# Performance work log

Measured on AMD Instinct MI355X. Metric: run time of the kernel, lower is better.

## Reference

```python
import jax, jax.numpy as jnp
import numpy as np

N, D, K = 32768, 128, 32
EPS = 1e-8  # torch.cosine_similarity default eps


def setup_inputs() -> dict:
    key = jax.random.key(0)
    k1, k2, k3, k4, k5 = jax.random.split(key, 5)
    # xavier_normal_ std = sqrt(2/(fan_in+fan_out)); torch treats dims (-2,-1) as (fan_in, fan_out)
    std_w = (2.0 / (D + D)) ** 0.5
    std_v = (2.0 / (2 * D + 1)) ** 0.5
    return {
        "x_1": jax.random.normal(k1, (N, D), dtype=jnp.float32),
        "x_2": jax.random.normal(k2, (N, D), dtype=jnp.float32),
        "W1": jax.random.normal(k3, (K, D, D), dtype=jnp.float32) * std_w,
        "W2": jax.random.normal(k4, (K, D, D), dtype=jnp.float32) * std_w,
        "V": jax.random.normal(k5, (K, 2 * D, 1), dtype=jnp.float32) * std_v,
        "b": jnp.zeros((K,), dtype=jnp.float32),
    }


def reference(x_1, x_2, W1, W2, V, b):
    # Batched bilinear transforms: [N, K, D]
    x1t = jnp.einsum("nd,kde->nke", x_1, W1)
    x2t = jnp.einsum("nd,kde->nke", x_2, W2)
    # Cosine similarity along last dim (torch semantics: clamp norms at eps)
    dot = jnp.sum(x1t * x2t, axis=-1)                     # [N, K]
    n1 = jnp.maximum(jnp.linalg.norm(x1t, axis=-1), EPS)  # [N, K]
    n2 = jnp.maximum(jnp.linalg.norm(x2t, axis=-1), EPS)
    part1 = dot / (n1 * n2)
    # part2 = cat([x1, x2]) @ V[k]  -> [N, K]
    xcat = jnp.concatenate([x_1, x_2], axis=-1)           # [N, 2D]
    part2 = jnp.einsum("nf,kf->nk", xcat, V[:, :, 0])
    return jax.nn.relu(part1 + part2 + b)
```

## Files before the change

kernel.cpp:

```cpp
#include <hip/hip_runtime.h>
#include <cstdint>
#include <cstddef>

#define DD 128
#define KK 32
constexpr float EPS = 1e-8f;

typedef __bf16 bf16x8 __attribute__((ext_vector_type(8)));
typedef float f32x4 __attribute__((ext_vector_type(4)));

__device__ __forceinline__ unsigned short f2bf(float x) {
    union { float f; uint32_t u; } v; v.f = x;
    uint32_t r = v.u + 0x7FFFu + ((v.u >> 16) & 1u);
    return (unsigned short)(r >> 16);
}
__device__ __forceinline__ __bf16 f2bf16(float x) {
    unsigned short u = f2bf(x);
    __bf16 r; __builtin_memcpy(&r, &u, 2); return r;
}
__device__ __forceinline__ uint4 pack8(float4 a, float4 b) {
    uint4 o;
    o.x = (uint32_t)f2bf(a.x) | ((uint32_t)f2bf(a.y) << 16);
    o.y = (uint32_t)f2bf(a.z) | ((uint32_t)f2bf(a.w) << 16);
    o.z = (uint32_t)f2bf(b.x) | ((uint32_t)f2bf(b.y) << 16);
    o.w = (uint32_t)f2bf(b.z) | ((uint32_t)f2bf(b.w) << 16);
    return o;
}

template <int CTRL>
__device__ __forceinline__ float dpp_fold(float x) {
    union { float f; int i; } u, r;
    u.f = x;
    r.i = __builtin_amdgcn_update_dpp(0, u.i, CTRL, 0xF, 0xF, false);
    return x + r.f;
}
__device__ __forceinline__ f32x4 fold4(f32x4 v) {
    #pragma unroll
    for (int c = 0; c < 4; ++c) {
        float x = v[c];
        x = dpp_fold<0xB1>(x);
        x = dpp_fold<0x4E>(x);
        v[c] = x;
    }
    return v;
}

__global__ __launch_bounds__(256) void prep_kernel(
    const float* __restrict__ x1, const float* __restrict__ x2,
    const float* __restrict__ W1, const float* __restrict__ W2,
    __bf16* __restrict__ X1f, __bf16* __restrict__ X2f,
    __bf16* __restrict__ W1f, __bf16* __restrict__ W2f,
    int cvt_half, int wf_half)
{
    __shared__ float tile[16][132];
    int bb = blockIdx.x;
    if (bb < 2 * cvt_half) {
        const float* src; __bf16* dst;
        if (bb >= cvt_half) { src = x2; dst = X2f; bb -= cvt_half; }
        else                { src = x1; dst = X1f; }
        const int rg = bb;
        {
            const int row = threadIdx.x >> 4;
            const int c8  = (threadIdx.x & 15) * 8;
            const float* p = src + (size_t)(rg * 16 + row) * DD + c8;
            float4 f0 = *reinterpret_cast<const float4*>(p);
            float4 f1 = *reinterpret_cast<const float4*>(p + 4);
            *reinterpret_cast<float4*>(&tile[row][c8])     = f0;
            *reinterpret_cast<float4*>(&tile[row][c8 + 4]) = f1;
        }
        __syncthreads();
        {
            const int mm = threadIdx.x & 15;
            const int c  = threadIdx.x >> 4;
            float4 a = *reinterpret_cast<float4*>(&tile[mm][c * 8]);
            float4 b = *reinterpret_cast<float4*>(&tile[mm][c * 8 + 4]);
            size_t off = (size_t)rg * 2048 + (size_t)c * 128 + (size_t)mm * 8;
            *reinterpret_cast<uint4*>(dst + off) = pack8(a, b);
        }
    } else {
        bb -= 2 * cvt_half;
        const float* W; __bf16* Wf;
        if (bb >= wf_half) { W = W2; Wf = W2f; bb -= wf_half; }
        else               { W = W1; Wf = W1f; }
        int idx = bb * 256 + threadIdx.x;
        int mm = idx & 15;
        int c  = (idx >> 4) & 15;
        int eg = (idx >> 8) & 7;
        int k  = idx >> 11;
        const float* Wk = W + (size_t)k * DD * DD;
        int e = eg * 16 + mm;
        float4 a, b;
        a.x = Wk[(size_t)(c * 8 + 0) * DD + e];
        a.y = Wk[(size_t)(c * 8 + 1) * DD + e];
        a.z = Wk[(size_t)(c * 8 + 2) * DD + e];
        a.w = Wk[(size_t)(c * 8 + 3) * DD + e];
        b.x = Wk[(size_t)(c * 8 + 4) * DD + e];
        b.y = Wk[(size_t)(c * 8 + 5) * DD + e];
        b.z = Wk[(size_t)(c * 8 + 6) * DD + e];
        b.w = Wk[(size_t)(c * 8 + 7) * DD + e];
        size_t off = ((size_t)(k * 8 + eg)) * 2048 + (size_t)c * 128 + (size_t)mm * 8;
        *reinterpret_cast<uint4*>(Wf + off) = pack8(a, b);
    }
}

__global__ __launch_bounds__(256) void part2_kernel(
    const __bf16* __restrict__ X1f, const __bf16* __restrict__ X2f,
    const float* __restrict__ V, float* __restrict__ p2w) {
    const int wave = threadIdx.x >> 6, lane = threadIdx.x & 63;
    const int m = lane & 15, quad = lane >> 4;
    const int rg0 = blockIdx.x * 16 + wave * 4;

    f32x4 acc[4][2];
    #pragma unroll
    for (int rt = 0; rt < 4; ++rt)
        #pragma unroll
        for (int ct = 0; ct < 2; ++ct) acc[rt][ct] = f32x4{0.f, 0.f, 0.f, 0.f};

    #pragma unroll
    for (int ks = 0; ks < 8; ++ks) {
        const __bf16* Xs = (ks < 4) ? X1f : X2f;
        const int kss = ks & 3;
        bf16x8 a[4];
        #pragma unroll
        for (int rt = 0; rt < 4; ++rt)
            a[rt] = *reinterpret_cast<const bf16x8*>(
                Xs + (size_t)(rg0 + rt) * 2048 + kss * 512 + lane * 8);
        #pragma unroll
        for (int ct = 0; ct < 2; ++ct) {
            const float* p = V + (size_t)(ct * 16 + m) * 256 + ks * 32 + quad * 8;
            float4 v0 = *reinterpret_cast<const float4*>(p);
            float4 v1 = *reinterpret_cast<const float4*>(p + 4);
            bf16x8 b;
            b[0] = f2bf16(v0.x); b[1] = f2bf16(v0.y); b[2] = f2bf16(v0.z); b[3] = f2bf16(v0.w);
            b[4] = f2bf16(v1.x); b[5] = f2bf16(v1.y); b[6] = f2bf16(v1.z); b[7] = f2bf16(v1.w);
            #pragma unroll
            for (int rt = 0; rt < 4; ++rt)
                acc[rt][ct] = __builtin_amdgcn_mfma_f32_16x16x32_bf16(a[rt], b, acc[rt][ct], 0, 0, 0);
        }
    }
    const int row0 = blockIdx.x * 256 + wave * 64;
    #pragma unroll
    for (int rt = 0; rt < 4; ++rt)
        #pragma unroll
        for (int ct = 0; ct < 2; ++ct)
            #pragma unroll
            for (int reg = 0; reg < 4; ++reg)
                p2w[(size_t)(row0 + rt * 16 + quad * 4 + reg) * KK + ct * 16 + m] = acc[rt][ct][reg];
}

__global__ __launch_bounds__(256, 2) void ntn_main(
    const __bf16* __restrict__ X1f, const __bf16* __restrict__ X2f,
    const __bf16* __restrict__ W1f, const __bf16* __restrict__ W2f,
    const float* __restrict__ p2w, const float* __restrict__ bias,
    float* __restrict__ out, int grp_per_xcd)
{
    __shared__ __align__(16) float sRedAll[8][3][2][4][40];

    const int b    = blockIdx.x;
    const int xcd  = b & 7;
    const int k    = (b >> 3) & 31;
    const int grpN = xcd * grp_per_xcd + (b >> 8);
    const int tid  = threadIdx.x;
    const int wave = tid >> 6;
    const int lane = tid & 63;
    const int m    = lane & 15;
    const int quad = lane >> 4;
    const int rh   = wave & 1;
    const int eh   = wave >> 1;

    const size_t nOut = (size_t)grpN * 256 + tid;
    const float p2v = p2w[nOut * KK + k];
    const float bk  = bias[k];

    const __bf16* W1p = W1f + (size_t)k * 16384;
    const __bf16* W2p = W2f + (size_t)k * 16384;

    bf16x8 Bc[2][4][4];
    #pragma unroll
    for (int ks = 0; ks < 4; ++ks)
        #pragma unroll
        for (int et = 0; et < 4; ++et) {
            const size_t boff = (size_t)(eh * 4 + et) * 2048 + ks * 512 + lane * 8;
            Bc[0][ks][et] = *reinterpret_cast<const bf16x8*>(W1p + boff);
            Bc[1][ks][et] = *reinterpret_cast<const bf16x8*>(W2p + boff);
        }

    const int rg0 = grpN * 16;
    const size_t lane8 = (size_t)lane * 8;

    bf16x8 a1[4], a2[4];
    {
        const size_t ab = (size_t)(rg0 + rh) * 2048 + lane8;
        #pragma unroll
        for (int ks = 0; ks < 4; ++ks) {
            a1[ks] = *reinterpret_cast<const bf16x8*>(X1f + ab + ks * 512);
            a2[ks] = *reinterpret_cast<const bf16x8*>(X2f + ab + ks * 512);
        }
    }

    #pragma unroll
    for (int g = 0; g < 8; ++g) {
        f32x4 acc[2][4];
        #pragma unroll
        for (int mat = 0; mat < 2; ++mat)
            #pragma unroll
            for (int et = 0; et < 4; ++et) acc[mat][et] = f32x4{0.f, 0.f, 0.f, 0.f};

        #pragma unroll
        for (int ks = 0; ks < 4; ++ks) {
            #pragma unroll
            for (int et = 0; et < 4; ++et) {
                acc[0][et] = __builtin_amdgcn_mfma_f32_16x16x32_bf16(a1[ks], Bc[0][ks][et], acc[0][et], 0, 0, 0);
                acc[1][et] = __builtin_amdgcn_mfma_f32_16x16x32_bf16(a2[ks], Bc[1][ks][et], acc[1][et], 0, 0, 0);
            }
        }

        if (g < 7) {
            const size_t ab = (size_t)(rg0 + (g + 1) * 2 + rh) * 2048 + lane8;
            #pragma unroll
            for (int ks = 0; ks < 4; ++ks) {
                a1[ks] = *reinterpret_cast<const bf16x8*>(X1f + ab + ks * 512);
                a2[ks] = *reinterpret_cast<const bf16x8*>(X2f + ab + ks * 512);
            }
        }

        f32x4 pd = {0.f, 0.f, 0.f, 0.f};
        f32x4 q1 = {0.f, 0.f, 0.f, 0.f};
        f32x4 q2 = {0.f, 0.f, 0.f, 0.f};
        #pragma unroll
        for (int et = 0; et < 4; ++et) {
            f32x4 c1 = acc[0][et];
            f32x4 c2 = acc[1][et];
            pd += c1 * c2;
            q1 += c1 * c1;
            q2 += c2 * c2;
        }
        pd = fold4(pd);
        q1 = fold4(q1);
        q2 = fold4(q2);

        if ((m & 3) == 0) {
            const int grp = m >> 2;
            const int rb  = rh * 16 + quad * 4;
            *reinterpret_cast<f32x4*>(&sRedAll[g][0][eh][grp][rb]) = pd;
            *reinterpret_cast<f32x4*>(&sRedAll[g][1][eh][grp][rb]) = q1;
            *reinterpret_cast<f32x4*>(&sRedAll[g][2][eh][grp][rb]) = q2;
        }
    }

    __syncthreads();

    {
        const int tile = tid >> 5;
        const int row  = tid & 31;
        float dot = 0.f, s1 = 0.f, s2 = 0.f;
        #pragma unroll
        for (int e2 = 0; e2 < 2; ++e2)
            #pragma unroll
            for (int gg = 0; gg < 4; ++gg) {
                dot += sRedAll[tile][0][e2][gg][row];
                s1  += sRedAll[tile][1][e2][gg][row];
                s2  += sRedAll[tile][2][e2][gg][row];
            }
        float n1 = fmaxf(sqrtf(s1), EPS);
        float n2 = fmaxf(sqrtf(s2), EPS);
        float tot = dot / (n1 * n2) + p2v + bk;
        out[nOut * KK + k] = fmaxf(tot, 0.f);
    }
}

extern "C" void kernel_launch(void* const* d_in, const int* in_sizes, int n_in,
                              void* d_out, int out_size, void* d_ws, size_t ws_size,
                              hipStream_t stream) {
    const float* x1 = (const float*)d_in[0];
    const float* x2 = (const float*)d_in[1];
    const float* W1 = (const float*)d_in[2];
    const float* W2 = (const float*)d_in[3];
    const float* V  = (const float*)d_in[4];
    const float* b  = (const float*)d_in[5];
    float* out = (float*)d_out;

    const int N = in_sizes[0] / DD;

    __bf16* X1f = (__bf16*)d_ws;
    __bf16* X2f = X1f + (size_t)N * DD;
    __bf16* W1f = X2f + (size_t)N * DD;
    __bf16* W2f = W1f + (size_t)KK * DD * DD;
    float*  p2w = (float*)(W2f + (size_t)KK * DD * DD);

    const int cvt_half = N / 16;
    const int wf_half  = KK * DD * DD / 8 / 256;
    prep_kernel<<<2 * cvt_half + 2 * wf_half, 256, 0, stream>>>(
        x1, x2, W1, W2, X1f, X2f, W1f, W2f, cvt_half, wf_half);

    part2_kernel<<<N / 256, 256, 0, stream>>>(X1f, X2f, V, p2w);

    const int groups = N / 256;
    ntn_main<<<groups * KK, 256, 0, stream>>>(X1f, X2f, W1f, W2f, p2w, b, out,
                                              groups / 8);
}
```

Measured before the change: 170.0 us.

## Fold part2 GEMV into prep kernel and raise MFMA wave priority

Removes the separate bf16 MFMA part2 kernel and computes the x·V projection as an fp32 GEMV inside the prep kernel, using extra blocks that read the raw fp32 inputs. This saves one kernel launch and removes the dependency of part2 on the bf16 conversion. The trade-off is that x1/x2 are now read twice in fp32 within prep and the GEMV runs on scalar FMAs instead of MFMA. Separately, it wraps the main kernel's MFMA loop in s_setprio to favour waves that are issuing matrix work.

```diff
diff --git a/kernel.cpp b/kernel.cpp
--- a/kernel.cpp
+++ b/kernel.cpp
@@ -13,10 +13,6 @@
     union { float f; uint32_t u; } v; v.f = x;
     uint32_t r = v.u + 0x7FFFu + ((v.u >> 16) & 1u);
     return (unsigned short)(r >> 16);
-}
-__device__ __forceinline__ __bf16 f2bf16(float x) {
-    unsigned short u = f2bf(x);
-    __bf16 r; __builtin_memcpy(&r, &u, 2); return r;
 }
 __device__ __forceinline__ uint4 pack8(float4 a, float4 b) {
     uint4 o;
@@ -48,20 +44,54 @@
 __global__ __launch_bounds__(256) void prep_kernel(
     const float* __restrict__ x1, const float* __restrict__ x2,
     const float* __restrict__ W1, const float* __restrict__ W2,
+    const float* __restrict__ V,  float* __restrict__ p2w,
     __bf16* __restrict__ X1f, __bf16* __restrict__ X2f,
     __bf16* __restrict__ W1f, __bf16* __restrict__ W2f,
-    int cvt_half, int wf_half)
+    int ngemv, int cvt_half, int wf_half)
 {
     __shared__ float tile[16][132];
+    __shared__ float xrow[8][260];
+
     int bb = blockIdx.x;
+    const int tid = threadIdx.x;
+
+    if (bb < ngemv) {
+        const int rb = bb * 8;
+        #pragma unroll
+        for (int i = 0; i < 2; ++i) {
+            int idx = tid + i * 256;
+            int row = idx >> 6;
+            int col = idx & 63;
+            const float* src = (col < 32)
+                ? (x1 + (size_t)(rb + row) * DD + col * 4)
+                : (x2 + (size_t)(rb + row) * DD + (col - 32) * 4);
+            *reinterpret_cast<float4*>(&xrow[row][col * 4]) =
+                *reinterpret_cast<const float4*>(src);
+        }
+        __syncthreads();
+        const int k   = tid & 31;
+        const int row = tid >> 5;
+        const float* Vk = V + (size_t)k * 256;
+        float acc = 0.f;
+        #pragma unroll 8
+        for (int c = 0; c < 64; ++c) {
+            float4 v  = *reinterpret_cast<const float4*>(Vk + c * 4);
+            float4 xv = *reinterpret_cast<const float4*>(&xrow[row][c * 4]);
+            acc += xv.x * v.x + xv.y * v.y + xv.z * v.z + xv.w * v.w;
+        }
+        p2w[(size_t)(rb + row) * KK + k] = acc;
+        return;
+    }
+    bb -= ngemv;
+
     if (bb < 2 * cvt_half) {
         const float* src; __bf16* dst;
         if (bb >= cvt_half) { src = x2; dst = X2f; bb -= cvt_half; }
         else                { src = x1; dst = X1f; }
         const int rg = bb;
         {
-            const int row = threadIdx.x >> 4;
-            const int c8  = (threadIdx.x & 15) * 8;
+            const int row = tid >> 4;
+            const int c8  = (tid & 15) * 8;
             const float* p = src + (size_t)(rg * 16 + row) * DD + c8;
             float4 f0 = *reinterpret_cast<const float4*>(p);
             float4 f1 = *reinterpret_cast<const float4*>(p + 4);
@@ -70,8 +100,8 @@
         }
         __syncthreads();
         {
-            const int mm = threadIdx.x & 15;
-            const int c  = threadIdx.x >> 4;
+            const int mm = tid & 15;
+            const int c  = tid >> 4;
             float4 a = *reinterpret_cast<float4*>(&tile[mm][c * 8]);
             float4 b = *reinterpret_cast<float4*>(&tile[mm][c * 8 + 4]);
             size_t off = (size_t)rg * 2048 + (size_t)c * 128 + (size_t)mm * 8;
@@ -82,7 +112,7 @@
         const float* W; __bf16* Wf;
         if (bb >= wf_half) { W = W2; Wf = W2f; bb -= wf_half; }
         else               { W = W1; Wf = W1f; }
-        int idx = bb * 256 + threadIdx.x;
+        int idx = bb * 256 + tid;
         int mm = idx & 15;
         int c  = (idx >> 4) & 15;
         int eg = (idx >> 8) & 7;
@@ -103,51 +133,6 @@
     }
 }
 
-__global__ __launch_bounds__(256) void part2_kernel(
-    const __bf16* __restrict__ X1f, const __bf16* __restrict__ X2f,
-    const float* __restrict__ V, float* __restrict__ p2w) {
-    const int wave = threadIdx.x >> 6, lane = threadIdx.x & 63;
-    const int m = lane & 15, quad = lane >> 4;
-    const int rg0 = blockIdx.x * 16 + wave * 4;
-
-    f32x4 acc[4][2];
-    #pragma unroll
-    for (int rt = 0; rt < 4; ++rt)
-        #pragma unroll
-        for (int ct = 0; ct < 2; ++ct) acc[rt][ct] = f32x4{0.f, 0.f, 0.f, 0.f};
-
-    #pragma unroll
-    for (int ks = 0; ks < 8; ++ks) {
-        const __bf16* Xs = (ks < 4) ? X1f : X2f;
-        const int kss = ks & 3;
-        bf16x8 a[4];
-        #pragma unroll
-        for (int rt = 0; rt < 4; ++rt)
-            a[rt] = *reinterpret_cast<const bf16x8*>(
-                Xs + (size_t)(rg0 + rt) * 2048 + kss * 512 + lane * 8);
-        #pragma unroll
-        for (int ct = 0; ct < 2; ++ct) {
-            const float* p = V + (size_t)(ct * 16 + m) * 256 + ks * 32 + quad * 8;
-            float4 v0 = *reinterpret_cast<const float4*>(p);
-            float4 v1 = *reinterpret_cast<const float4*>(p + 4);
-            bf16x8 b;
-            b[0] = f2bf16(v0.x); b[1] = f2bf16(v0.y); b[2] = f2bf16(v0.z); b[3] = f2bf16(v0.w);
-            b[4] = f2bf16(v1.x); b[5] = f2bf16(v1.y); b[6] = f2bf16(v1.z); b[7] = f2bf16(v1.w);
-            #pragma unroll
-            for (int rt = 0; rt < 4; ++rt)
-                acc[rt][ct] = __builtin_amdgcn_mfma_f32_16x16x32_bf16(a[rt], b, acc[rt][ct], 0, 0, 0);
-        }
-    }
-    const int row0 = blockIdx.x * 256 + wave * 64;
-    #pragma unroll
-    for (int rt = 0; rt < 4; ++rt)
-        #pragma unroll
-        for (int ct = 0; ct < 2; ++ct)
-            #pragma unroll
-            for (int reg = 0; reg < 4; ++reg)
-                p2w[(size_t)(row0 + rt * 16 + quad * 4 + reg) * KK + ct * 16 + m] = acc[rt][ct][reg];
-}
-
 __global__ __launch_bounds__(256, 2) void ntn_main(
     const __bf16* __restrict__ X1f, const __bf16* __restrict__ X2f,
     const __bf16* __restrict__ W1f, const __bf16* __restrict__ W2f,
@@ -206,6 +191,7 @@
             #pragma unroll
             for (int et = 0; et < 4; ++et) acc[mat][et] = f32x4{0.f, 0.f, 0.f, 0.f};
 
+        __builtin_amdgcn_s_setprio(1);
         #pragma unroll
         for (int ks = 0; ks < 4; ++ks) {
             #pragma unroll
@@ -214,6 +200,7 @@
                 acc[1][et] = __builtin_amdgcn_mfma_f32_16x16x32_bf16(a2[ks], Bc[1][ks][et], acc[1][et], 0, 0, 0);
             }
         }
+        __builtin_amdgcn_s_setprio(0);
 
         if (g < 7) {
             const size_t ab = (size_t)(rg0 + (g + 1) * 2 + rh) * 2048 + lane8;
@@ -288,12 +275,11 @@
     __bf16* W2f = W1f + (size_t)KK * DD * DD;
     float*  p2w = (float*)(W2f + (size_t)KK * DD * DD);
 
+    const int ngemv    = N / 8;
     const int cvt_half = N / 16;
     const int wf_half  = KK * DD * DD / 8 / 256;
-    prep_kernel<<<2 * cvt_half + 2 * wf_half, 256, 0, stream>>>(
-        x1, x2, W1, W2, X1f, X2f, W1f, W2f, cvt_half, wf_half);
-
-    part2_kernel<<<N / 256, 256, 0, stream>>>(X1f, X2f, V, p2w);
+    prep_kernel<<<ngemv + 2 * cvt_half + 2 * wf_half, 256, 0, stream>>>(
+        x1, x2, W1, W2, V, p2w, X1f, X2f, W1f, W2f, ngemv, cvt_half, wf_half);
 
     const int groups = N / 256;
     ntn_main<<<groups * KK, 256, 0, stream>>>(X1f, X2f, W1f, W2f, p2w, b, out,
```

Measured after the change: 271.9 us. +60.0%, slower.

## Fuse part2 linear term into main NTN kernel via extra MFMAs

Applied to the files above, without the earlier changes.

Drops the separate part2 kernel and its p2w workspace round trip. Each wave in the main kernel now computes the V projection with four extra MFMAs per row group, using a B operand in which only column 0 is non-zero, so 15 of 16 MFMA columns are wasted. Each half of the e split covers its own x1 or x2 half, and the two halves are summed through shared memory in the epilogue. It also raises wave priority around the MFMA section with s_setprio, and pays extra register use and redundant MFMA work in each of the 32 k-blocks to save one launch and the global write and read.

```diff
diff --git a/kernel.cpp b/kernel.cpp
--- a/kernel.cpp
+++ b/kernel.cpp
@@ -103,58 +103,14 @@
     }
 }
 
-__global__ __launch_bounds__(256) void part2_kernel(
-    const __bf16* __restrict__ X1f, const __bf16* __restrict__ X2f,
-    const float* __restrict__ V, float* __restrict__ p2w) {
-    const int wave = threadIdx.x >> 6, lane = threadIdx.x & 63;
-    const int m = lane & 15, quad = lane >> 4;
-    const int rg0 = blockIdx.x * 16 + wave * 4;
-
-    f32x4 acc[4][2];
-    #pragma unroll
-    for (int rt = 0; rt < 4; ++rt)
-        #pragma unroll
-        for (int ct = 0; ct < 2; ++ct) acc[rt][ct] = f32x4{0.f, 0.f, 0.f, 0.f};
-
-    #pragma unroll
-    for (int ks = 0; ks < 8; ++ks) {
-        const __bf16* Xs = (ks < 4) ? X1f : X2f;
-        const int kss = ks & 3;
-        bf16x8 a[4];
-        #pragma unroll
-        for (int rt = 0; rt < 4; ++rt)
-            a[rt] = *reinterpret_cast<const bf16x8*>(
-                Xs + (size_t)(rg0 + rt) * 2048 + kss * 512 + lane * 8);
-        #pragma unroll
-        for (int ct = 0; ct < 2; ++ct) {
-            const float* p = V + (size_t)(ct * 16 + m) * 256 + ks * 32 + quad * 8;
-            float4 v0 = *reinterpret_cast<const float4*>(p);
-            float4 v1 = *reinterpret_cast<const float4*>(p + 4);
-            bf16x8 b;
-            b[0] = f2bf16(v0.x); b[1] = f2bf16(v0.y); b[2] = f2bf16(v0.z); b[3] = f2bf16(v0.w);
-            b[4] = f2bf16(v1.x); b[5] = f2bf16(v1.y); b[6] = f2bf16(v1.z); b[7] = f2bf16(v1.w);
-            #pragma unroll
-            for (int rt = 0; rt < 4; ++rt)
-                acc[rt][ct] = __builtin_amdgcn_mfma_f32_16x16x32_bf16(a[rt], b, acc[rt][ct], 0, 0, 0);
-        }
-    }
-    const int row0 = blockIdx.x * 256 + wave * 64;
-    #pragma unroll
-    for (int rt = 0; rt < 4; ++rt)
-        #pragma unroll
-        for (int ct = 0; ct < 2; ++ct)
-            #pragma unroll
-            for (int reg = 0; reg < 4; ++reg)
-                p2w[(size_t)(row0 + rt * 16 + quad * 4 + reg) * KK + ct * 16 + m] = acc[rt][ct][reg];
-}
-
 __global__ __launch_bounds__(256, 2) void ntn_main(
     const __bf16* __restrict__ X1f, const __bf16* __restrict__ X2f,
     const __bf16* __restrict__ W1f, const __bf16* __restrict__ W2f,
-    const float* __restrict__ p2w, const float* __restrict__ bias,
+    const float* __restrict__ V, const float* __restrict__ bias,
     float* __restrict__ out, int grp_per_xcd)
 {
     __shared__ __align__(16) float sRedAll[8][3][2][4][40];
+    __shared__ __align__(16) float sP2[8][2][2][16];
 
     const int b    = blockIdx.x;
     const int xcd  = b & 7;
@@ -169,7 +125,6 @@
     const int eh   = wave >> 1;
 
     const size_t nOut = (size_t)grpN * 256 + tid;
-    const float p2v = p2w[nOut * KK + k];
     const float bk  = bias[k];
 
     const __bf16* W1p = W1f + (size_t)k * 16384;
@@ -185,6 +140,26 @@
             Bc[1][ks][et] = *reinterpret_cast<const bf16x8*>(W2p + boff);
         }
 
+    bf16x8 Vb[4];
+    {
+        const float* Vk = V + (size_t)k * 256 + eh * 128 + quad * 8;
+        #pragma unroll
+        for (int ks = 0; ks < 4; ++ks) {
+            float4 v0 = *reinterpret_cast<const float4*>(Vk + ks * 32);
+            float4 v1 = *reinterpret_cast<const float4*>(Vk + ks * 32 + 4);
+            bf16x8 t;
+            t[0] = f2bf16(v0.x); t[1] = f2bf16(v0.y);
+            t[2] = f2bf16(v0.z); t[3] = f2bf16(v0.w);
+            t[4] = f2bf16(v1.x); t[5] = f2bf16(v1.y);
+            t[6] = f2bf16(v1.z); t[7] = f2bf16(v1.w);
+            if (m != 0) {
+                #pragma unroll
+                for (int j = 0; j < 8; ++j) t[j] = (__bf16)0.0f;
+            }
+            Vb[ks] = t;
+        }
+    }
+
     const int rg0 = grpN * 16;
     const size_t lane8 = (size_t)lane * 8;
 
@@ -205,7 +180,9 @@
         for (int mat = 0; mat < 2; ++mat)
             #pragma unroll
             for (int et = 0; et < 4; ++et) acc[mat][et] = f32x4{0.f, 0.f, 0.f, 0.f};
-
+        f32x4 accv = {0.f, 0.f, 0.f, 0.f};
+
+        __builtin_amdgcn_s_setprio(1);
         #pragma unroll
         for (int ks = 0; ks < 4; ++ks) {
             #pragma unroll
@@ -214,6 +191,16 @@
                 acc[1][et] = __builtin_amdgcn_mfma_f32_16x16x32_bf16(a2[ks], Bc[1][ks][et], acc[1][et], 0, 0, 0);
             }
         }
+        if (eh == 0) {
+            #pragma unroll
+            for (int ks = 0; ks < 4; ++ks)
+                accv = __builtin_amdgcn_mfma_f32_16x16x32_bf16(a1[ks], Vb[ks], accv, 0, 0, 0);
+        } else {
+            #pragma unroll
+            for (int ks = 0; ks < 4; ++ks)
+                accv = __builtin_amdgcn_mfma_f32_16x16x32_bf16(a2[ks], Vb[ks], accv, 0, 0, 0);
+        }
+        __builtin_amdgcn_s_setprio(0);
 
         if (g < 7) {
             const size_t ab = (size_t)(rg0 + (g + 1) * 2 + rh) * 2048 + lane8;
@@ -246,6 +233,9 @@
             *reinterpret_cast<f32x4*>(&sRedAll[g][1][eh][grp][rb]) = q1;
             *reinterpret_cast<f32x4*>(&sRedAll[g][2][eh][grp][rb]) = q2;
         }
+        if (m == 0) {
+            *reinterpret_cast<f32x4*>(&sP2[g][eh][rh][quad * 4]) = accv;
+        }
     }
 
     __syncthreads();
@@ -253,6 +243,8 @@
     {
         const int tile = tid >> 5;
         const int row  = tid & 31;
+        const int rowh = row >> 4;
+        const int rowl = row & 15;
         float dot = 0.f, s1 = 0.f, s2 = 0.f;
         #pragma unroll
         for (int e2 = 0; e2 < 2; ++e2)
@@ -262,6 +254,7 @@
                 s1  += sRedAll[tile][1][e2][gg][row];
                 s2  += sRedAll[tile][2][e2][gg][row];
             }
+        float p2v = sP2[tile][0][rowh][rowl] + sP2[tile][1][rowh][rowl];
         float n1 = fmaxf(sqrtf(s1), EPS);
         float n2 = fmaxf(sqrtf(s2), EPS);
         float tot = dot / (n1 * n2) + p2v + bk;
@@ -286,16 +279,13 @@
     __bf16* X2f = X1f + (size_t)N * DD;
     __bf16* W1f = X2f + (size_t)N * DD;
     __bf16* W2f = W1f + (size_t)KK * DD * DD;
-    float*  p2w = (float*)(W2f + (size_t)KK * DD * DD);
 
     const int cvt_half = N / 16;
     const int wf_half  = KK * DD * DD / 8 / 256;
     prep_kernel<<<2 * cvt_half + 2 * wf_half, 256, 0, stream>>>(
         x1, x2, W1, W2, X1f, X2f, W1f, W2f, cvt_half, wf_half);
 
-    part2_kernel<<<N / 256, 256, 0, stream>>>(X1f, X2f, V, p2w);
-
     const int groups = N / 256;
-    ntn_main<<<groups * KK, 256, 0, stream>>>(X1f, X2f, W1f, W2f, p2w, b, out,
+    ntn_main<<<groups * KK, 256, 0, stream>>>(X1f, X2f, W1f, W2f, V, b, out,
                                               groups / 8);
 }
```

Result: no change. 167.6 us (-1.4%).
